# Kernel tuning notes

Measured on AMD Instinct MI355X. Metric: run time of the kernel, lower is better.

Reference implementation:

```python
import jax, jax.numpy as jnp
import numpy as np

EMBED_DIM = 512
NUM_HEADS = 8
QKV_DIM = 64
MS_HIDDEN = 16
COST_DIMS = 1
SCORES_DIMS = COST_DIMS + 1  # dot-product score + cost-mat score


def setup_inputs() -> dict:
    key = jax.random.key(0)
    ks = jax.random.split(key, 12)
    B, R, C = 8, 256, 256
    row_emb = jax.random.normal(ks[0], (B, R, EMBED_DIM), dtype=jnp.float32)
    col_emb = jax.random.normal(ks[1], (B, C, EMBED_DIM), dtype=jnp.float32)
    cost_mat = jax.random.uniform(ks[2], (B, R, C, COST_DIMS), dtype=jnp.float32)
    attn_mask = jax.random.randint(ks[3], (B, R, C), 0, 2).astype(jnp.bool_)
    # learned params (stored [in, out]; torch Linear applies x @ W.T)
    s = 1.0 / np.sqrt(EMBED_DIM)
    Wq = jax.random.uniform(ks[4], (EMBED_DIM, NUM_HEADS * QKV_DIM), minval=-s, maxval=s)
    Wk = jax.random.uniform(ks[5], (EMBED_DIM, NUM_HEADS * QKV_DIM), minval=-s, maxval=s)
    Wv = jax.random.uniform(ks[6], (EMBED_DIM, NUM_HEADS * QKV_DIM), minval=-s, maxval=s)
    Wo = jax.random.uniform(ks[7], (EMBED_DIM, EMBED_DIM), minval=-s, maxval=s)
    m1 = np.sqrt(1.0 / SCORES_DIMS)
    m2 = np.sqrt(1.0 / MS_HIDDEN)
    W1 = jax.random.uniform(ks[8], (SCORES_DIMS * NUM_HEADS, MS_HIDDEN * NUM_HEADS), minval=-m1, maxval=m1)
    W2 = jax.random.uniform(ks[9], (MS_HIDDEN * NUM_HEADS, NUM_HEADS), minval=-m2, maxval=m2)
    alpha = jnp.ones((1, NUM_HEADS, 1, 1, 1), dtype=jnp.float32)
    return {"row_emb": row_emb, "col_emb": col_emb, "cost_mat": cost_mat,
            "attn_mask": attn_mask, "Wq": Wq, "Wk": Wk, "Wv": Wv, "Wo": Wo,
            "W1": W1, "W2": W2, "alpha": alpha}


def reference(row_emb, col_emb, cost_mat, attn_mask, Wq, Wk, Wv, Wo, W1, W2, alpha):
    B, R, E = row_emb.shape
    C = col_emb.shape[1]
    H, D = NUM_HEADS, QKV_DIM
    norm = 1.0 / jnp.sqrt(jnp.asarray(D, row_emb.dtype))
    # projections -> (b, h, s, d)
    q = (row_emb @ Wq).reshape(B, R, H, D).transpose(0, 2, 1, 3)
    k = (col_emb @ Wk).reshape(B, C, H, D).transpose(0, 2, 1, 3)
    v = (col_emb @ Wv).reshape(B, C, H, D).transpose(0, 2, 1, 3)
    dot = norm * jnp.einsum('bhrd,bhcd->bhrc', q, k)  # (B,H,R,C)
    # mixed-score MLP: concat dot score with alpha-scaled cost-mat score
    cm = alpha * cost_mat[:, None]                    # (B,H,R,C,COST_DIMS)
    scores = jnp.concatenate([dot[..., None], cm], axis=-1)  # (B,H,R,C,S)
    s = scores.transpose(0, 2, 3, 1, 4).reshape(B, R, C, H * SCORES_DIMS)
    mixed = jax.nn.relu(s @ W1) @ W2                  # (B,R,C,H)
    logits = mixed.transpose(0, 3, 1, 2)              # (B,H,R,C)
    # masked softmax (rows fully masked -> zero weights)
    mask = attn_mask[:, None]                         # (B,1,R,C)
    all_masked = jnp.all(mask, axis=-1, keepdims=True)
    logits = jnp.where(mask, -jnp.inf, logits)
    weights = jax.nn.softmax(logits, axis=-1)
    weights = jnp.where(all_masked, 0.0, weights)
    out = jnp.einsum('bhrc,bhcd->bhrd', weights, v)   # (B,H,R,D)
    out = out.transpose(0, 2, 1, 3).reshape(B, R, H * D)
    return out @ Wo
```

## Files before the change

### kernel.cpp

```cpp
#include <hip/hip_runtime.h>
#include <hip/hip_bf16.h>

#define B_ 8
#define R_ 256
#define C_ 256
#define H_ 8
#define D_ 64

typedef __attribute__((ext_vector_type(8))) short s8v;
typedef __attribute__((ext_vector_type(4))) short s4v;
typedef __attribute__((ext_vector_type(4))) float f4v;

static __device__ __forceinline__ unsigned short f2b(float x) {
    __hip_bfloat16 h = __float2bfloat16(x);
    return *reinterpret_cast<unsigned short*>(&h);
}
static __device__ __forceinline__ float b2f(unsigned short u) {
    union { unsigned int i; float f; } c;
    c.i = (unsigned int)u << 16;
    return c.f;
}

__global__ __launch_bounds__(256) void prep(
    const float* __restrict__ re, const float* __restrict__ ce,
    const float* __restrict__ W1, const float* __restrict__ W2,
    const float* __restrict__ alpha,
    unsigned short* __restrict__ reb, unsigned short* __restrict__ ceb,
    unsigned short* __restrict__ w1af, unsigned short* __restrict__ w2af)
{
    const int t = blockIdx.x * 256 + threadIdx.x;
    {
        float2 v = *(const float2*)&re[(size_t)t * 2];
        reb[t * 2]     = f2b(v.x);
        reb[t * 2 + 1] = f2b(v.y);
        float2 w = *(const float2*)&ce[(size_t)t * 2];
        ceb[t * 2]     = f2b(w.x);
        ceb[t * 2 + 1] = f2b(w.y);
    }
    if (blockIdx.x == 0) {
        const int l = threadIdx.x;
        for (int q = 0; q < 16; ++q) {
            const int idx = l * 16 + q;
            const int kk = idx & 7, lane = (idx >> 3) & 63, n = idx >> 9;
            const int j = n * 16 + (lane & 15);
            const int s = 8 * (lane >> 4) + kk;
            float val = 0.f;
            if (s < 16) {
                val = W1[(2 * (s >> 1)) * 128 + j];
            } else if (s < 18) {
                for (int h = 0; h < 8; ++h)
                    val += alpha[h] * W1[(2 * h + 1) * 128 + j];
            }
            w1af[idx] = f2b(val);
        }
        for (int q = 0; q < 8; ++q) {
            const int idx = l * 8 + q;
            const int kk = idx & 7, lane = (idx >> 3) & 63, kc = idx >> 9;
            const int h = lane & 15, g = lane >> 4;
            const int phi = 16 * (2 * kc + (kk >> 2)) + 4 * g + (kk & 3);
            w2af[idx] = f2b(h < 8 ? W2[phi * 8 + h] : 0.f);
        }
    }
}

__global__ __launch_bounds__(256) void prep_w(
    const float* __restrict__ Wq, const float* __restrict__ Wk,
    const float* __restrict__ Wv, const float* __restrict__ Wo,
    unsigned short* __restrict__ wqt, unsigned short* __restrict__ wkt,
    unsigned short* __restrict__ wvt, unsigned short* __restrict__ wot)
{
    __shared__ unsigned short ldsT[64][68];
    const int which = blockIdx.y;
    const float* W = which == 0 ? Wq : which == 1 ? Wk : which == 2 ? Wv : Wo;
    unsigned short* WT = which == 0 ? wqt : which == 1 ? wkt : which == 2 ? wvt : wot;
    const int k0 = (blockIdx.x & 7) * 64;
    const int n0 = (blockIdx.x >> 3) * 64;
    const int t = threadIdx.x;
    const int rn = t & 15;
    const int rk = t >> 4;
    #pragma unroll
    for (int i = 0; i < 4; ++i) {
        const int kk = rk + 16 * i;
        const float4 v = *(const float4*)&W[(size_t)(k0 + kk) * 512 + n0 + rn * 4];
        ldsT[rn * 4 + 0][kk] = f2b(v.x);
        ldsT[rn * 4 + 1][kk] = f2b(v.y);
        ldsT[rn * 4 + 2][kk] = f2b(v.z);
        ldsT[rn * 4 + 3][kk] = f2b(v.w);
    }
    __syncthreads();
    #pragma unroll
    for (int i = 0; i < 4; ++i) {
        const int nn = rk + 16 * i;
        const s4v r = *(const s4v*)&ldsT[nn][rn * 4];
        *(s4v*)&WT[(size_t)(n0 + nn) * 512 + k0 + rn * 4] = r;
    }
}

__global__ __launch_bounds__(256) void gemm_qkv(
    const unsigned short* __restrict__ reb, const unsigned short* __restrict__ ceb,
    const unsigned short* __restrict__ wqt, const unsigned short* __restrict__ wkt,
    const unsigned short* __restrict__ wvt,
    unsigned short* __restrict__ Qb, unsigned short* __restrict__ Kb,
    unsigned short* __restrict__ VT)
{
    const int z = blockIdx.z;
    const unsigned short* A;
    const unsigned short* Bm;
    int Ar0, Br0;
    if (z == 0)      { A = reb; Bm = wqt; Ar0 = blockIdx.x * 64; Br0 = blockIdx.y * 64; }
    else if (z == 1) { A = ceb; Bm = wkt; Ar0 = blockIdx.x * 64; Br0 = blockIdx.y * 64; }
    else             { A = wvt; Bm = ceb; Ar0 = blockIdx.y * 64; Br0 = blockIdx.x * 64; }

    const int t = threadIdx.x, lane = t & 63, wave = t >> 6;
    const int row0 = Ar0 + (wave >> 1) * 32;
    const int col0 = Br0 + (wave & 1) * 32;
    const int lr = lane & 15, ko = (lane >> 4) * 8;

    const unsigned short* Ap0 = A + (size_t)(row0 + lr) * 512 + ko;
    const unsigned short* Ap1 = Ap0 + 16 * 512;
    const unsigned short* Bp0 = Bm + (size_t)(col0 + lr) * 512 + ko;
    const unsigned short* Bp1 = Bp0 + 16 * 512;

    f4v acc[2][2] = {};
    #pragma unroll 4
    for (int k0 = 0; k0 < 512; k0 += 32) {
        s8v a0 = *(const s8v*)(Ap0 + k0);
        s8v a1 = *(const s8v*)(Ap1 + k0);
        s8v b0 = *(const s8v*)(Bp0 + k0);
        s8v b1 = *(const s8v*)(Bp1 + k0);
        acc[0][0] = __builtin_amdgcn_mfma_f32_16x16x32_bf16(a0, b0, acc[0][0], 0, 0, 0);
        acc[0][1] = __builtin_amdgcn_mfma_f32_16x16x32_bf16(a0, b1, acc[0][1], 0, 0, 0);
        acc[1][0] = __builtin_amdgcn_mfma_f32_16x16x32_bf16(a1, b0, acc[1][0], 0, 0, 0);
        acc[1][1] = __builtin_amdgcn_mfma_f32_16x16x32_bf16(a1, b1, acc[1][1], 0, 0, 0);
    }

    const float sc = (z == 0) ? 0.125f : 1.0f;
    const int rbase = (lane >> 4) * 4;
    #pragma unroll
    for (int i = 0; i < 2; ++i)
        #pragma unroll
        for (int j = 0; j < 2; ++j)
            #pragma unroll
            for (int reg = 0; reg < 4; ++reg) {
                const int rowIdx = row0 + i * 16 + rbase + reg;
                const int colIdx = col0 + j * 16 + lr;
                const unsigned short v = f2b(acc[i][j][reg] * sc);
                if (z == 0) {
                    Qb[(size_t)rowIdx * 512 + colIdx] = v;
                } else if (z == 1) {
                    const int b = rowIdx >> 8, c = rowIdx & 255;
                    const int h = colIdx >> 6, d = colIdx & 63;
                    Kb[(((size_t)b * 8 + h) * 256 + c) * 64 + d] = v;
                } else {
                    const int h = rowIdx >> 6, d = rowIdx & 63;
                    const int b = colIdx >> 8, c = colIdx & 255;
                    VT[(((size_t)b * 8 + h) * 64 + d) * 256 + c] = v;
                }
            }
}

__global__ __launch_bounds__(256) void gemm_out(
    const unsigned short* __restrict__ OHb, const unsigned short* __restrict__ wot,
    float* __restrict__ out)
{
    const int t = threadIdx.x, lane = t & 63, wave = t >> 6;
    const int row0 = blockIdx.x * 64 + (wave >> 1) * 32;
    const int col0 = blockIdx.y * 64 + (wave & 1) * 32;
    const int lr = lane & 15, ko = (lane >> 4) * 8;

    const unsigned short* Ap0 = OHb + (size_t)(row0 + lr) * 512 + ko;
    const unsigned short* Ap1 = Ap0 + 16 * 512;
    const unsigned short* Bp0 = wot + (size_t)(col0 + lr) * 512 + ko;
    const unsigned short* Bp1 = Bp0 + 16 * 512;

    f4v acc[2][2] = {};
    #pragma unroll 4
    for (int k0 = 0; k0 < 512; k0 += 32) {
        s8v a0 = *(const s8v*)(Ap0 + k0);
        s8v a1 = *(const s8v*)(Ap1 + k0);
        s8v b0 = *(const s8v*)(Bp0 + k0);
        s8v b1 = *(const s8v*)(Bp1 + k0);
        acc[0][0] = __builtin_amdgcn_mfma_f32_16x16x32_bf16(a0, b0, acc[0][0], 0, 0, 0);
        acc[0][1] = __builtin_amdgcn_mfma_f32_16x16x32_bf16(a0, b1, acc[0][1], 0, 0, 0);
        acc[1][0] = __builtin_amdgcn_mfma_f32_16x16x32_bf16(a1, b0, acc[1][0], 0, 0, 0);
        acc[1][1] = __builtin_amdgcn_mfma_f32_16x16x32_bf16(a1, b1, acc[1][1], 0, 0, 0);
    }

    const int rbase = (lane >> 4) * 4;
    #pragma unroll
    for (int i = 0; i < 2; ++i)
        #pragma unroll
        for (int j = 0; j < 2; ++j)
            #pragma unroll
            for (int reg = 0; reg < 4; ++reg)
                out[(size_t)(row0 + i * 16 + rbase + reg) * 512 + col0 + j * 16 + lr] =
                    acc[i][j][reg];
}

__global__ __launch_bounds__(512, 2) void attn_fused(
    const unsigned short* __restrict__ Qb,
    const unsigned short* __restrict__ Kb,
    const unsigned short* __restrict__ VT,
    const float* __restrict__ cost,
    const int* __restrict__ mask,
    const unsigned short* __restrict__ w1af,
    const unsigned short* __restrict__ w2af,
    unsigned short* __restrict__ OHb)
{
    __shared__ unsigned short dotb[4][256][24];
    __shared__ unsigned short w_t3[8][4][264];

    const int t    = threadIdx.x;
    const int lane = t & 63;
    const int w    = t >> 6;
    const int li   = lane & 15;
    const int g    = lane >> 4;
    const int b    = blockIdx.y;
    const int r0   = blockIdx.x * 4;

    {
        const int rr = lane & 3;
        const int ko = g * 8;
        const unsigned short* Qp = Qb + ((size_t)b * R_ + r0 + rr) * 512 + w * 64 + ko;
        const s8v a0 = *(const s8v*)Qp;
        const s8v a1 = *(const s8v*)(Qp + 32);
        const unsigned short* Kp = Kb + (((size_t)b * 8 + w) * 256) * 64;
        #pragma unroll
        for (int ct = 0; ct < 16; ++ct) {
            const unsigned short* Bp = Kp + (size_t)(ct * 16 + li) * 64 + ko;
            const s8v b0 = *(const s8v*)Bp;
            const s8v b1v = *(const s8v*)(Bp + 32);
            f4v acc = __builtin_amdgcn_mfma_f32_16x16x32_bf16(a0, b0, (f4v){0.f,0.f,0.f,0.f}, 0, 0, 0);
            acc = __builtin_amdgcn_mfma_f32_16x16x32_bf16(a1, b1v, acc, 0, 0, 0);
            if (lane < 16) {
                const int c = ct * 16 + lane;
                #pragma unroll
                for (int reg = 0; reg < 4; ++reg) {
                    const float x = acc[reg];
                    const unsigned short hi = f2b(x);
                    const unsigned short lo = f2b(x - b2f(hi));
                    *(unsigned int*)&dotb[reg][c][2 * w] =
                        (unsigned int)hi | ((unsigned int)lo << 16);
                }
            }
        }
    }
    __syncthreads();

    {
        s8v w1A[8], w2A[4];
        #pragma unroll
        for (int n = 0; n < 8; ++n) w1A[n] = ((const s8v*)w1af)[n * 64 + lane];
        #pragma unroll
        for (int kc = 0; kc < 4; ++kc) w2A[kc] = ((const s8v*)w2af)[kc * 64 + lane];

        const int r   = w & 3;
        const int ct0 = (w >> 2) * 8;
        const float* costRow = cost + ((size_t)b * R_ + r0 + r) * 256;

        #pragma unroll
        for (int i = 0; i < 8; ++i) {
            const int c = (ct0 + i) * 16 + li;
            s8v b1;
            {
                const s8v t0 = *(const s8v*)&dotb[r][c][(g & 1) * 8];
                const float cv = costRow[c];
                const unsigned short chi = f2b(cv);
                const unsigned short clo = f2b(cv - b2f(chi));
                if (g < 2) {
                    b1 = t0;
                } else if (g == 2) {
                    s8v bc = {0, 0, 0, 0, 0, 0, 0, 0};
                    bc[0] = (short)chi; bc[1] = (short)clo;
                    b1 = bc;
                } else {
                    s8v bz = {0, 0, 0, 0, 0, 0, 0, 0};
                    b1 = bz;
                }
            }
            unsigned int pk[16];
            #pragma unroll
            for (int n = 0; n < 8; ++n) {
                f4v acc = __builtin_amdgcn_mfma_f32_16x16x32_bf16(
                    w1A[n], b1, (f4v){0.f,0.f,0.f,0.f}, 0, 0, 0);
                const float a0 = fmaxf(acc[0], 0.f), a1 = fmaxf(acc[1], 0.f);
                const float a2 = fmaxf(acc[2], 0.f), a3 = fmaxf(acc[3], 0.f);
                pk[2 * n]     = (unsigned int)f2b(a0) | ((unsigned int)f2b(a1) << 16);
                pk[2 * n + 1] = (unsigned int)f2b(a2) | ((unsigned int)f2b(a3) << 16);
            }
            f4v acc2 = (f4v){0.f, 0.f, 0.f, 0.f};
            #pragma unroll
            for (int kc = 0; kc < 4; ++kc) {
                union { s8v v; unsigned int u[4]; } bb;
                bb.u[0] = pk[4 * kc + 0];
                bb.u[1] = pk[4 * kc + 1];
                bb.u[2] = pk[4 * kc + 2];
                bb.u[3] = pk[4 * kc + 3];
                acc2 = __builtin_amdgcn_mfma_f32_16x16x32_bf16(w2A[kc], bb.v, acc2, 0, 0, 0);
            }
            if (g < 2) {
                float* lp = (float*)&dotb[r][c][0];
                #pragma unroll
                for (int reg = 0; reg < 4; ++reg)
                    lp[4 * g + reg] = acc2[reg];
            }
        }
    }
    __syncthreads();

    {
        #pragma unroll
        for (int p = 0; p < 4; ++p) {
            const int idx = w * 4 + p;
            const int r = idx >> 3, h = idx & 7;
            const int4 mk = *(const int4*)&mask[((size_t)b * R_ + r0 + r) * 256 + lane * 4];
            float v[4];
            #pragma unroll
            for (int i = 0; i < 4; ++i)
                v[i] = ((const float*)&dotb[r][lane * 4 + i][0])[h];
            const bool m0 = mk.x != 0, m1 = mk.y != 0;
            const bool m2 = mk.z != 0, m3 = mk.w != 0;
            const float v0 = m0 ? -INFINITY : v[0];
            const float v1 = m1 ? -INFINITY : v[1];
            const float v2 = m2 ? -INFINITY : v[2];
            const float v3 = m3 ? -INFINITY : v[3];
            float mx = fmaxf(fmaxf(v0, v1), fmaxf(v2, v3));
            #pragma unroll
            for (int off = 32; off >= 1; off >>= 1)
                mx = fmaxf(mx, __shfl_xor(mx, off));
            const float e0 = m0 ? 0.f : __expf(v0 - mx);
            const float e1 = m1 ? 0.f : __expf(v1 - mx);
            const float e2 = m2 ? 0.f : __expf(v2 - mx);
            const float e3 = m3 ? 0.f : __expf(v3 - mx);
            float sm = e0 + e1 + e2 + e3;
            #pragma unroll
            for (int off = 32; off >= 1; off >>= 1)
                sm += __shfl_xor(sm, off);
            const float inv = sm > 0.f ? 1.0f / sm : 0.f;
            s4v pk;
            pk[0] = (short)f2b(e0 * inv);
            pk[1] = (short)f2b(e1 * inv);
            pk[2] = (short)f2b(e2 * inv);
            pk[3] = (short)f2b(e3 * inv);
            *(s4v*)&w_t3[h][r][lane * 4] = pk;
        }
    }
    __syncthreads();

    {
        s8v bfr[8];
        #pragma unroll
        for (int kt = 0; kt < 8; ++kt)
            bfr[kt] = *(const s8v*)&w_t3[w][li & 3][kt * 32 + g * 8];
        const unsigned short* Vp = VT + (((size_t)b * 8 + w) * 64) * 256;
        #pragma unroll
        for (int dt = 0; dt < 4; ++dt) {
            const unsigned short* Ap = Vp + (size_t)(dt * 16 + li) * 256 + g * 8;
            f4v acc = (f4v){0.f, 0.f, 0.f, 0.f};
            #pragma unroll
            for (int kt = 0; kt < 8; ++kt)
                acc = __builtin_amdgcn_mfma_f32_16x16x32_bf16(
                    *(const s8v*)(Ap + kt * 32), bfr[kt], acc, 0, 0, 0);
            if (li < 4) {
                s4v o;
                o[0] = (short)f2b(acc[0]);
                o[1] = (short)f2b(acc[1]);
                o[2] = (short)f2b(acc[2]);
                o[3] = (short)f2b(acc[3]);
                *(s4v*)&OHb[((size_t)b * R_ + r0 + li) * 512 + w * 64 + dt * 16 + 4 * g] = o;
            }
        }
    }
}

extern "C" void kernel_launch(void* const* d_in, const int* in_sizes, int n_in,
                              void* d_out, int out_size, void* d_ws, size_t ws_size,
                              hipStream_t stream)
{
    const float* row_emb = (const float*)d_in[0];
    const float* col_emb = (const float*)d_in[1];
    const float* cost    = (const float*)d_in[2];
    const int*   mask    = (const int*)d_in[3];
    const float* Wq = (const float*)d_in[4];
    const float* Wk = (const float*)d_in[5];
    const float* Wv = (const float*)d_in[6];
    const float* Wo = (const float*)d_in[7];
    const float* W1 = (const float*)d_in[8];
    const float* W2 = (const float*)d_in[9];
    const float* alpha = (const float*)d_in[10];
    float* out = (float*)d_out;

    unsigned short* base = (unsigned short*)d_ws;
    unsigned short* Qb   = base;
    unsigned short* Kb   = base + 1048576;
    unsigned short* VT   = base + 2097152;
    unsigned short* OHb  = base + 3145728;
    unsigned short* reb  = base + 4194304;
    unsigned short* ceb  = base + 5242880;
    unsigned short* wqt  = base + 6291456;
    unsigned short* wkt  = base + 6553600;
    unsigned short* wvt  = base + 6815744;
    unsigned short* wot  = base + 7077888;
    unsigned short* w1af = base + 7340032;
    unsigned short* w2af = base + 7344128;

    prep<<<2048, 256, 0, stream>>>(row_emb, col_emb, W1, W2, alpha,
                                   reb, ceb, w1af, w2af);
    prep_w<<<dim3(64, 4), 256, 0, stream>>>(Wq, Wk, Wv, Wo, wqt, wkt, wvt, wot);
    gemm_qkv<<<dim3(32, 8, 3), 256, 0, stream>>>(reb, ceb, wqt, wkt, wvt,
                                                 Qb, Kb, VT);
    attn_fused<<<dim3(64, 8), 512, 0, stream>>>(Qb, Kb, VT, cost, mask,
                                                w1af, w2af, OHb);
    gemm_out<<<dim3(32, 8), 256, 0, stream>>>(OHb, wot, out);
}
```

Baseline: 93.37 us.

## Halve rows per attention block, stage MLP weights in LDS, merge prep kernels

```diff
diff --git a/kernel.cpp b/kernel.cpp
--- a/kernel.cpp
+++ b/kernel.cpp
@@ -25,9 +25,43 @@
     const float* __restrict__ re, const float* __restrict__ ce,
     const float* __restrict__ W1, const float* __restrict__ W2,
     const float* __restrict__ alpha,
+    const float* __restrict__ Wq, const float* __restrict__ Wk,
+    const float* __restrict__ Wv, const float* __restrict__ Wo,
     unsigned short* __restrict__ reb, unsigned short* __restrict__ ceb,
-    unsigned short* __restrict__ w1af, unsigned short* __restrict__ w2af)
+    unsigned short* __restrict__ w1af, unsigned short* __restrict__ w2af,
+    unsigned short* __restrict__ wqt, unsigned short* __restrict__ wkt,
+    unsigned short* __restrict__ wvt, unsigned short* __restrict__ wot)
 {
+    __shared__ unsigned short ldsT[64][68];
+    if (blockIdx.x >= 2048) {
+        const int bb = blockIdx.x - 2048;
+        const int which = bb >> 6;
+        const float* W = which == 0 ? Wq : which == 1 ? Wk : which == 2 ? Wv : Wo;
+        unsigned short* WT = which == 0 ? wqt : which == 1 ? wkt : which == 2 ? wvt : wot;
+        const int k0 = (bb & 7) * 64;
+        const int n0 = ((bb >> 3) & 7) * 64;
+        const int tt = threadIdx.x;
+        const int rn = tt & 15;
+        const int rk = tt >> 4;
+        #pragma unroll
+        for (int i = 0; i < 4; ++i) {
+            const int kk = rk + 16 * i;
+            const float4 v = *(const float4*)&W[(size_t)(k0 + kk) * 512 + n0 + rn * 4];
+            ldsT[rn * 4 + 0][kk] = f2b(v.x);
+            ldsT[rn * 4 + 1][kk] = f2b(v.y);
+            ldsT[rn * 4 + 2][kk] = f2b(v.z);
+            ldsT[rn * 4 + 3][kk] = f2b(v.w);
+        }
+        __syncthreads();
+        #pragma unroll
+        for (int i = 0; i < 4; ++i) {
+            const int nn = rk + 16 * i;
+            const s4v r = *(const s4v*)&ldsT[nn][rn * 4];
+            *(s4v*)&WT[(size_t)(n0 + nn) * 512 + k0 + rn * 4] = r;
+        }
+        return;
+    }
+
     const int t = blockIdx.x * 256 + threadIdx.x;
     {
         float2 v = *(const float2*)&re[(size_t)t * 2];
@@ -60,39 +94,6 @@
             const int phi = 16 * (2 * kc + (kk >> 2)) + 4 * g + (kk & 3);
             w2af[idx] = f2b(h < 8 ? W2[phi * 8 + h] : 0.f);
         }
-    }
-}
-
-__global__ __launch_bounds__(256) void prep_w(
-    const float* __restrict__ Wq, const float* __restrict__ Wk,
-    const float* __restrict__ Wv, const float* __restrict__ Wo,
-    unsigned short* __restrict__ wqt, unsigned short* __restrict__ wkt,
-    unsigned short* __restrict__ wvt, unsigned short* __restrict__ wot)
-{
-    __shared__ unsigned short ldsT[64][68];
-    const int which = blockIdx.y;
-    const float* W = which == 0 ? Wq : which == 1 ? Wk : which == 2 ? Wv : Wo;
-    unsigned short* WT = which == 0 ? wqt : which == 1 ? wkt : which == 2 ? wvt : wot;
-    const int k0 = (blockIdx.x & 7) * 64;
-    const int n0 = (blockIdx.x >> 3) * 64;
-    const int t = threadIdx.x;
-    const int rn = t & 15;
-    const int rk = t >> 4;
-    #pragma unroll
-    for (int i = 0; i < 4; ++i) {
-        const int kk = rk + 16 * i;
-        const float4 v = *(const float4*)&W[(size_t)(k0 + kk) * 512 + n0 + rn * 4];
-        ldsT[rn * 4 + 0][kk] = f2b(v.x);
-        ldsT[rn * 4 + 1][kk] = f2b(v.y);
-        ldsT[rn * 4 + 2][kk] = f2b(v.z);
-        ldsT[rn * 4 + 3][kk] = f2b(v.w);
-    }
-    __syncthreads();
-    #pragma unroll
-    for (int i = 0; i < 4; ++i) {
-        const int nn = rk + 16 * i;
-        const s4v r = *(const s4v*)&ldsT[nn][rn * 4];
-        *(s4v*)&WT[(size_t)(n0 + nn) * 512 + k0 + rn * 4] = r;
     }
 }
 
@@ -197,7 +198,7 @@
                     acc[i][j][reg];
 }
 
-__global__ __launch_bounds__(512, 2) void attn_fused(
+__global__ __launch_bounds__(512, 8) void attn_fused(
     const unsigned short* __restrict__ Qb,
     const unsigned short* __restrict__ Kb,
     const unsigned short* __restrict__ VT,
@@ -207,8 +208,10 @@
     const unsigned short* __restrict__ w2af,
     unsigned short* __restrict__ OHb)
 {
-    __shared__ unsigned short dotb[4][256][24];
-    __shared__ unsigned short w_t3[8][4][264];
+    __shared__ unsigned short dotb[2][256][16];
+    __shared__ unsigned short w_t3[8][2][264];
+    __shared__ unsigned short ws1[4096];
+    __shared__ unsigned short ws2[2048];
 
     const int t    = threadIdx.x;
     const int lane = t & 63;
@@ -216,10 +219,13 @@
     const int li   = lane & 15;
     const int g    = lane >> 4;
     const int b    = blockIdx.y;
-    const int r0   = blockIdx.x * 4;
+    const int r0   = blockIdx.x * 2;
+
+    ((s8v*)ws1)[t] = ((const s8v*)w1af)[t];
+    if (t < 256) ((s8v*)ws2)[t] = ((const s8v*)w2af)[t];
 
     {
-        const int rr = lane & 3;
+        const int rr = lane & 1;
         const int ko = g * 8;
         const unsigned short* Qp = Qb + ((size_t)b * R_ + r0 + rr) * 512 + w * 64 + ko;
         const s8v a0 = *(const s8v*)Qp;
@@ -235,7 +241,7 @@
             if (lane < 16) {
                 const int c = ct * 16 + lane;
                 #pragma unroll
-                for (int reg = 0; reg < 4; ++reg) {
+                for (int reg = 0; reg < 2; ++reg) {
                     const float x = acc[reg];
                     const unsigned short hi = f2b(x);
                     const unsigned short lo = f2b(x - b2f(hi));
@@ -248,18 +254,12 @@
     __syncthreads();
 
     {
-        s8v w1A[8], w2A[4];
-        #pragma unroll
-        for (int n = 0; n < 8; ++n) w1A[n] = ((const s8v*)w1af)[n * 64 + lane];
-        #pragma unroll
-        for (int kc = 0; kc < 4; ++kc) w2A[kc] = ((const s8v*)w2af)[kc * 64 + lane];
-
-        const int r   = w & 3;
-        const int ct0 = (w >> 2) * 8;
+        const int r   = w & 1;
+        const int ct0 = (w >> 1) * 4;
         const float* costRow = cost + ((size_t)b * R_ + r0 + r) * 256;
 
         #pragma unroll
-        for (int i = 0; i < 8; ++i) {
+        for (int i = 0; i < 4; ++i) {
             const int c = (ct0 + i) * 16 + li;
             s8v b1;
             {
@@ -281,8 +281,9 @@
             unsigned int pk[16];
             #pragma unroll
             for (int n = 0; n < 8; ++n) {
+                const s8v w1A = *(const s8v*)&ws1[(n * 64 + lane) * 8];
                 f4v acc = __builtin_amdgcn_mfma_f32_16x16x32_bf16(
-                    w1A[n], b1, (f4v){0.f,0.f,0.f,0.f}, 0, 0, 0);
+                    w1A, b1, (f4v){0.f,0.f,0.f,0.f}, 0, 0, 0);
                 const float a0 = fmaxf(acc[0], 0.f), a1 = fmaxf(acc[1], 0.f);
                 const float a2 = fmaxf(acc[2], 0.f), a3 = fmaxf(acc[3], 0.f);
                 pk[2 * n]     = (unsigned int)f2b(a0) | ((unsigned int)f2b(a1) << 16);
@@ -291,12 +292,13 @@
             f4v acc2 = (f4v){0.f, 0.f, 0.f, 0.f};
             #pragma unroll
             for (int kc = 0; kc < 4; ++kc) {
+                const s8v w2A = *(const s8v*)&ws2[(kc * 64 + lane) * 8];
                 union { s8v v; unsigned int u[4]; } bb;
                 bb.u[0] = pk[4 * kc + 0];
                 bb.u[1] = pk[4 * kc + 1];
                 bb.u[2] = pk[4 * kc + 2];
                 bb.u[3] = pk[4 * kc + 3];
-                acc2 = __builtin_amdgcn_mfma_f32_16x16x32_bf16(w2A[kc], bb.v, acc2, 0, 0, 0);
+                acc2 = __builtin_amdgcn_mfma_f32_16x16x32_bf16(w2A, bb.v, acc2, 0, 0, 0);
             }
             if (g < 2) {
                 float* lp = (float*)&dotb[r][c][0];
@@ -310,39 +312,36 @@
 
     {
         #pragma unroll
-        for (int p = 0; p < 4; ++p) {
-            const int idx = w * 4 + p;
-            const int r = idx >> 3, h = idx & 7;
-            const int4 mk = *(const int4*)&mask[((size_t)b * R_ + r0 + r) * 256 + lane * 4];
+        for (int p = 0; p < 2; ++p) {
+            const int r = p, h = w;
+            const int* maskRow = mask + ((size_t)b * R_ + r0 + r) * 256;
             float v[4];
+            int mk[4];
+            #pragma unroll
+            for (int i = 0; i < 4; ++i) {
+                const int c = lane + 64 * i;
+                v[i]  = ((const float*)&dotb[r][c][0])[h];
+                mk[i] = maskRow[c];
+            }
             #pragma unroll
             for (int i = 0; i < 4; ++i)
-                v[i] = ((const float*)&dotb[r][lane * 4 + i][0])[h];
-            const bool m0 = mk.x != 0, m1 = mk.y != 0;
-            const bool m2 = mk.z != 0, m3 = mk.w != 0;
-            const float v0 = m0 ? -INFINITY : v[0];
-            const float v1 = m1 ? -INFINITY : v[1];
-            const float v2 = m2 ? -INFINITY : v[2];
-            const float v3 = m3 ? -INFINITY : v[3];
-            float mx = fmaxf(fmaxf(v0, v1), fmaxf(v2, v3));
+                v[i] = mk[i] ? -INFINITY : v[i];
+            float mx = fmaxf(fmaxf(v[0], v[1]), fmaxf(v[2], v[3]));
             #pragma unroll
             for (int off = 32; off >= 1; off >>= 1)
                 mx = fmaxf(mx, __shfl_xor(mx, off));
-            const float e0 = m0 ? 0.f : __expf(v0 - mx);
-            const float e1 = m1 ? 0.f : __expf(v1 - mx);
-            const float e2 = m2 ? 0.f : __expf(v2 - mx);
-            const float e3 = m3 ? 0.f : __expf(v3 - mx);
-            float sm = e0 + e1 + e2 + e3;
+            float e[4];
+            #pragma unroll
+            for (int i = 0; i < 4; ++i)
+                e[i] = mk[i] ? 0.f : __expf(v[i] - mx);
+            float sm = e[0] + e[1] + e[2] + e[3];
             #pragma unroll
             for (int off = 32; off >= 1; off >>= 1)
                 sm += __shfl_xor(sm, off);
             const float inv = sm > 0.f ? 1.0f / sm : 0.f;
-            s4v pk;
-            pk[0] = (short)f2b(e0 * inv);
-            pk[1] = (short)f2b(e1 * inv);
-            pk[2] = (short)f2b(e2 * inv);
-            pk[3] = (short)f2b(e3 * inv);
-            *(s4v*)&w_t3[h][r][lane * 4] = pk;
+            #pragma unroll
+            for (int i = 0; i < 4; ++i)
+                w_t3[h][r][lane + 64 * i] = f2b(e[i] * inv);
         }
     }
     __syncthreads();
@@ -351,7 +350,7 @@
         s8v bfr[8];
         #pragma unroll
         for (int kt = 0; kt < 8; ++kt)
-            bfr[kt] = *(const s8v*)&w_t3[w][li & 3][kt * 32 + g * 8];
+            bfr[kt] = *(const s8v*)&w_t3[w][li & 1][kt * 32 + g * 8];
         const unsigned short* Vp = VT + (((size_t)b * 8 + w) * 64) * 256;
         #pragma unroll
         for (int dt = 0; dt < 4; ++dt) {
@@ -361,7 +360,7 @@
             for (int kt = 0; kt < 8; ++kt)
                 acc = __builtin_amdgcn_mfma_f32_16x16x32_bf16(
                     *(const s8v*)(Ap + kt * 32), bfr[kt], acc, 0, 0, 0);
-            if (li < 4) {
+            if (li < 2) {
                 s4v o;
                 o[0] = (short)f2b(acc[0]);
                 o[1] = (short)f2b(acc[1]);
@@ -404,12 +403,12 @@
     unsigned short* w1af = base + 7340032;
     unsigned short* w2af = base + 7344128;
 
-    prep<<<2048, 256, 0, stream>>>(row_emb, col_emb, W1, W2, alpha,
-                                   reb, ceb, w1af, w2af);
-    prep_w<<<dim3(64, 4), 256, 0, stream>>>(Wq, Wk, Wv, Wo, wqt, wkt, wvt, wot);
+    prep<<<2304, 256, 0, stream>>>(row_emb, col_emb, W1, W2, alpha,
+                                   Wq, Wk, Wv, Wo,
+                                   reb, ceb, w1af, w2af, wqt, wkt, wvt, wot);
     gemm_qkv<<<dim3(32, 8, 3), 256, 0, stream>>>(reb, ceb, wqt, wkt, wvt,
                                                  Qb, Kb, VT);
-    attn_fused<<<dim3(64, 8), 512, 0, stream>>>(Qb, Kb, VT, cost, mask,
-                                                w1af, w2af, OHb);
+    attn_fused<<<dim3(128, 8), 512, 0, stream>>>(Qb, Kb, VT, cost, mask,
+                                                 w1af, w2af, OHb);
     gemm_out<<<dim3(32, 8), 256, 0, stream>>>(OHb, wot, out);
 }
```

Result: slower. 116.7 us (+25.0%).
